# Kernel tuning notes

Hardware: AMD Instinct MI355X
Metric: run time of the kernel (lower is better)

Reference implementation:

```python
import jax, jax.numpy as jnp
import numpy as np
from jax import lax

T, B, NIN, H, NOUT = 256, 64, 256, 2048, 256
DT, TAU, SIGMA = 20.0, 100.0, 0.05
DECAY = DT / TAU                      # alpha in the leaky-Euler update
NOISE_SCALE = SIGMA * float(np.sqrt(2.0 / DECAY))
MAX_INIT_STEPS = 100
ATOL = 0.1


def setup_inputs() -> dict:
    key = jax.random.key(0)
    k1, k2, k3, k4 = jax.random.split(key, 4)
    x = jax.random.normal(k1, (T, B, NIN), dtype=jnp.float32)
    W_ih = jax.random.normal(k2, (H, NIN), dtype=jnp.float32) / np.sqrt(NIN)
    # w_rec_init='diag': strong diagonal plus small random recurrent weights
    W_hh = 0.5 * jnp.eye(H, dtype=jnp.float32) + 0.1 * jax.random.normal(k3, (H, H), dtype=jnp.float32) / np.sqrt(H)
    b = jnp.zeros((H,), dtype=jnp.float32)
    W_out = jax.random.normal(k4, (NOUT, H), dtype=jnp.float32) / np.sqrt(H)
    return {"x": x, "W_ih": W_ih, "W_hh": W_hh, "b": b, "W_out": W_out}


def reference(x, W_ih, W_hh, b, W_out):
    base = jax.random.key(42)

    def cell(h, x_t, k):
        # leaky RNN step: h' = (1-a)h + a*relu(W_ih x + W_hh h + b + noise)
        pre = x_t @ W_ih.T + h @ W_hh.T + b
        pre = pre + NOISE_SCALE * jax.random.normal(k, pre.shape, dtype=pre.dtype)
        return (1.0 - DECAY) * h + DECAY * jax.nn.relu(pre)

    # ---- init_hidden_: up to 100 probe iterations of 2 steps on x[:2, 0:1] ----
    x_probe = x[:2, :1]                       # [2, 1, NIN], broadcasts vs h [B, H]
    h0_init = jnp.zeros((B, H), dtype=x.dtype)

    def init_body(carry, i):
        h0, stable, done = carry
        k = jax.random.fold_in(base, i)
        ka, kb = jax.random.split(k)
        h1 = cell(h0, x_probe[0], ka)
        h2 = cell(h1, x_probe[1], kb)
        close = jnp.max(jnp.abs(h2 - h0)) <= ATOL
        stable_new = jnp.where(done, stable, jnp.where(close, stable + 1, 0))
        trigger = (~done) & close & (stable_new >= 4)   # return pre-update h0
        done_new = done | trigger
        h0_new = jnp.where(done_new, h0, h2)
        return (h0_new, stable_new, done_new), None

    (h0, _, _), _ = lax.scan(init_body, (h0_init, jnp.int32(0), jnp.bool_(False)),
                             jnp.arange(MAX_INIT_STEPS))

    # ---- main unroll over T steps ----
    ks = jax.random.split(jax.random.fold_in(base, 1_000_000), T)

    def step(h, inp):
        x_t, k = inp
        h_new = cell(h, x_t, k)
        return h_new, h_new

    _, hidden = lax.scan(step, h0, (x, ks))   # [T, B, H]
    output = hidden @ W_out.T                 # [T, B, NOUT]
    return output, hidden
```

## Files before the change

kernel.cpp:

```cpp
#include <hip/hip_runtime.h>

typedef unsigned int u32;
typedef unsigned short u16;
typedef __bf16 bf16x8 __attribute__((ext_vector_type(8)));
typedef u16 us8 __attribute__((ext_vector_type(8)));
typedef u32 u32x4 __attribute__((ext_vector_type(4)));
typedef float f32x4 __attribute__((ext_vector_type(4)));

#define T_N 256
#define B_N 64
#define NIN_N 256
#define H_N 2048
#define NOUT_N 256
#define BH (B_N * H_N)
#define OUT_SZ (T_N * B_N * NOUT_N)

#define LDS_WHH_H 0
#define LDS_WHH_L 65536
#define LDS_RBUF  131072
#define LDS_RED   139264
#define LDS_BYTES 139328

struct U2 { u32 x, y; };

__device__ __forceinline__ u32 rotl32(u32 v, int r) { return (v << r) | (v >> (32 - r)); }

__device__ __forceinline__ U2 tf2x32(U2 k, U2 x) {
  u32 ks0 = k.x, ks1 = k.y, ks2 = k.x ^ k.y ^ 0x1BD11BDAu;
  x.x += ks0; x.y += ks1;
#define TFR(a) x.x += x.y; x.y = rotl32(x.y,(a)); x.y ^= x.x;
  TFR(13) TFR(15) TFR(26) TFR(6)
  x.x += ks1; x.y += ks2 + 1u;
  TFR(17) TFR(29) TFR(16) TFR(24)
  x.x += ks2; x.y += ks0 + 2u;
  TFR(13) TFR(15) TFR(26) TFR(6)
  x.x += ks0; x.y += ks1 + 3u;
  TFR(17) TFR(29) TFR(16) TFR(24)
  x.x += ks1; x.y += ks2 + 4u;
  TFR(13) TFR(15) TFR(26) TFR(6)
  x.x += ks2; x.y += ks0 + 5u;
#undef TFR
  return x;
}

__device__ __forceinline__ float jax_normal(u32 bits) {
  float f = __uint_as_float((bits >> 9) | 0x3f800000u) - 1.0f;
  const float lo = -0.99999994f;
  float u = fmaf(f, 2.0f, lo);
  u = fmaxf(u, lo);
  float w = -log1pf(-u * u);
  float p;
  if (w < 5.0f) {
    w = w - 2.5f;
    p =            2.81022636e-08f;
    p = fmaf(p, w, 3.43273939e-07f);
    p = fmaf(p, w, -3.5233877e-06f);
    p = fmaf(p, w, -4.39150654e-06f);
    p = fmaf(p, w, 0.00021858087f);
    p = fmaf(p, w, -0.00125372503f);
    p = fmaf(p, w, -0.00417768164f);
    p = fmaf(p, w, 0.246640727f);
    p = fmaf(p, w, 1.50140941f);
  } else {
    w = sqrtf(w) - 3.0f;
    p =            -0.000200214257f;
    p = fmaf(p, w, 0.000100950558f);
    p = fmaf(p, w, 0.00134934322f);
    p = fmaf(p, w, -0.00367342844f);
    p = fmaf(p, w, 0.00573950773f);
    p = fmaf(p, w, -0.0076224613f);
    p = fmaf(p, w, 0.00943887047f);
    p = fmaf(p, w, 1.00167406f);
    p = fmaf(p, w, 2.83297682f);
  }
  return 1.41421354f * (p * u);
}

__device__ __forceinline__ u16 f2bf(float f) {
  u32 x = __float_as_uint(f);
  u32 r = (x + 0x7FFFu + ((x >> 16) & 1u)) >> 16;
  return (u16)r;
}
__device__ __forceinline__ float bf2f(u16 b) { return __uint_as_float(((u32)b) << 16); }

__device__ __forceinline__ bf16x8 ld8(const u16* p) {
  us8 v = *reinterpret_cast<const us8*>(p);
  return __builtin_bit_cast(bf16x8, v);
}
__device__ __forceinline__ f32x4 mfma16(bf16x8 a, bf16x8 b, f32x4 c) {
  return __builtin_amdgcn_mfma_f32_16x16x32_bf16(a, b, c, 0, 0, 0);
}

__device__ __forceinline__ void st_agent_u16(u16* p, u16 v) {
  __hip_atomic_store(p, v, __ATOMIC_RELAXED, __HIP_MEMORY_SCOPE_AGENT);
}
__device__ __forceinline__ void st_agent_u32(u32* p, u32 v, int order) {
  if (order) __hip_atomic_store(p, v, __ATOMIC_RELEASE, __HIP_MEMORY_SCOPE_AGENT);
  else       __hip_atomic_store(p, v, __ATOMIC_RELAXED, __HIP_MEMORY_SCOPE_AGENT);
}
__device__ __forceinline__ u32 ld_agent_u32(const u32* p) {
  return __hip_atomic_load(p, __ATOMIC_RELAXED, __HIP_MEMORY_SCOPE_AGENT);
}

#define GLD16(AP, V) \
  asm volatile( \
    "global_load_dwordx4 %0, %16, off offset:-4096 sc0 sc1\n\t" \
    "global_load_dwordx4 %1, %16, off sc0 sc1\n\t" \
    "global_load_dwordx4 %2, %17, off offset:-4096 sc0 sc1\n\t" \
    "global_load_dwordx4 %3, %17, off sc0 sc1\n\t" \
    "global_load_dwordx4 %4, %18, off offset:-4096 sc0 sc1\n\t" \
    "global_load_dwordx4 %5, %18, off sc0 sc1\n\t" \
    "global_load_dwordx4 %6, %19, off offset:-4096 sc0 sc1\n\t" \
    "global_load_dwordx4 %7, %19, off sc0 sc1\n\t" \
    "global_load_dwordx4 %8, %20, off offset:-4096 sc0 sc1\n\t" \
    "global_load_dwordx4 %9, %20, off sc0 sc1\n\t" \
    "global_load_dwordx4 %10, %21, off offset:-4096 sc0 sc1\n\t" \
    "global_load_dwordx4 %11, %21, off sc0 sc1\n\t" \
    "global_load_dwordx4 %12, %22, off offset:-4096 sc0 sc1\n\t" \
    "global_load_dwordx4 %13, %22, off sc0 sc1\n\t" \
    "global_load_dwordx4 %14, %23, off offset:-4096 sc0 sc1\n\t" \
    "global_load_dwordx4 %15, %23, off sc0 sc1\n\t" \
    "s_waitcnt vmcnt(0)" \
    : "=&v"(V##0), "=&v"(V##1), "=&v"(V##2), "=&v"(V##3), \
      "=&v"(V##4), "=&v"(V##5), "=&v"(V##6), "=&v"(V##7), \
      "=&v"(V##8), "=&v"(V##9), "=&v"(V##10), "=&v"(V##11), \
      "=&v"(V##12), "=&v"(V##13), "=&v"(V##14), "=&v"(V##15) \
    : "v"(AP + 2048), "v"(AP + 3 * 2048), "v"(AP + 5 * 2048), "v"(AP + 7 * 2048), \
      "v"(AP + 9 * 2048), "v"(AP + 11 * 2048), "v"(AP + 13 * 2048), "v"(AP + 15 * 2048) \
    : "memory")

__global__ void __launch_bounds__(256) pack_b_kernel(const float* __restrict__ W,
    u16* __restrict__ hi, u16* __restrict__ lo, int K, int Cshift) {
  int tid = blockIdx.x * 256 + threadIdx.x;
  int lane = tid & 63;
  size_t tile = tid >> 6;
  int C = 1 << Cshift;
  int jt = (int)(tile >> Cshift), c = (int)(tile & (C - 1));
  int row = jt * 16 + (lane & 15);
  int k0 = c * 32 + (lane >> 4) * 8;
  const float* src = W + (size_t)row * K + k0;
  us8 vh, vl;
#pragma unroll
  for (int j = 0; j < 8; ++j) {
    float w = src[j];
    u16 hb = f2bf(w);
    vh[j] = hb;
    vl[j] = f2bf(w - bf2f(hb));
  }
  *reinterpret_cast<us8*>(hi + tile * 512 + lane * 8) = vh;
  *reinterpret_cast<us8*>(lo + tile * 512 + lane * 8) = vl;
}

__global__ void __launch_bounds__(256) pack_x_kernel(const float* __restrict__ x,
    u16* __restrict__ hi, u16* __restrict__ lo) {
  int tid = blockIdx.x * 256 + threadIdx.x;
  int t = tid >> 11;
  int r = tid & 2047;
  int lane = r & 63, piece = r >> 6;
  int c = piece >> 2, g = piece & 3;
  int row = g * 16 + (lane & 15);
  int k0 = c * 32 + (lane >> 4) * 8;
  const float* src = x + (size_t)t * (B_N * NIN_N) + (size_t)row * NIN_N + k0;
  us8 vh, vl;
#pragma unroll
  for (int j = 0; j < 8; ++j) {
    float w = src[j];
    u16 hb = f2bf(w);
    vh[j] = hb;
    vl[j] = f2bf(w - bf2f(hb));
  }
  size_t off = (size_t)t * 16384 + (size_t)piece * 512 + lane * 8;
  *reinterpret_cast<us8*>(hi + off) = vh;
  *reinterpret_cast<us8*>(lo + off) = vl;
}

__global__ void __launch_bounds__(256) probe_proj(const float* __restrict__ x,
    const float* __restrict__ Wih, const float* __restrict__ bias, float* __restrict__ xpj) {
  int g = blockIdx.x * 256 + threadIdx.x;
  int p = g >> 11, col = g & 2047;
  const float* xr = x + (size_t)p * (B_N * NIN_N);
  const float* wr = Wih + (size_t)col * NIN_N;
  float s = 0.f;
#pragma unroll 4
  for (int k = 0; k < NIN_N; ++k) s = fmaf(xr[k], wr[k], s);
  xpj[p * H_N + col] = s + bias[col];
}

__global__ void __launch_bounds__(256) xproj_gemm(const u16* __restrict__ xp_hi,
    const u16* __restrict__ xp_lo, const u16* __restrict__ wih_hi,
    const u16* __restrict__ wih_lo, const float* __restrict__ bias,
    float* __restrict__ xout) {
  int lane = threadIdx.x & 63, wvq = threadIdx.x >> 6;
  int t = blockIdx.x >> 7, jt16 = blockIdx.x & 127;
  const u16* ah = xp_hi + (size_t)t * 16384 + wvq * 512 + lane * 8;
  const u16* al = xp_lo + (size_t)t * 16384 + wvq * 512 + lane * 8;
  const u16* bh = wih_hi + (size_t)jt16 * 4096 + lane * 8;
  const u16* bl = wih_lo + (size_t)jt16 * 4096 + lane * 8;
  f32x4 z = {0.f, 0.f, 0.f, 0.f};
  f32x4 a0 = z, a1 = z, a2 = z;
#pragma unroll
  for (int c = 0; c < 8; ++c) {
    bf16x8 xh = ld8(ah + c * 2048), xl = ld8(al + c * 2048);
    bf16x8 wh = ld8(bh + c * 512),  wl = ld8(bl + c * 512);
    a0 = mfma16(xh, wh, a0);
    a1 = mfma16(xh, wl, a1);
    a2 = mfma16(xl, wh, a2);
  }
  f32x4 acc = (a0 + a1) + a2;
  int col = jt16 * 16 + (lane & 15);
  int q = lane >> 4;
  float bc = bias[col];
#pragma unroll
  for (int r = 0; r < 4; ++r) {
    int row = wvq * 16 + q * 4 + r;
    xout[(size_t)t * BH + (size_t)row * H_N + col] = acc[r] + bc;
  }
}

__global__ void setup_keys(U2* ka, U2* kb, U2* ks) {
  int i = threadIdx.x;
  U2 base{0u, 42u};
  if (i < 104) {
    U2 ki = tf2x32(base, U2{0u, (u32)i});
    ka[i] = tf2x32(ki, U2{0u, 0u});
    kb[i] = tf2x32(ki, U2{0u, 1u});
  }
  U2 km = tf2x32(base, U2{0u, 1000000u});
  ks[i] = tf2x32(km, U2{0u, (u32)i});
}

__global__ void __launch_bounds__(256) zero_bufs(u32* hx0w, u32* hx0lw, u32* bar) {
  int g = blockIdx.x * 256 + threadIdx.x;
  if (g < BH / 2) { hx0w[g] = 0u; hx0lw[g] = 0u; }
  if (g < 1024) bar[g] = 0u;
}

struct RnnParams {
  const u16 *whh_hi, *whh_lo;
  const float* xpj;
  float* hidden;
  u16 *hx0, *hx1, *hx2, *hxA, *hxB;
  u16 *hx0l, *hx1l, *hx2l;
  const U2 *ka, *kb, *ks;
  u32 *slots, *mslot;
};

__global__ void __launch_bounds__(512) rnn_persistent(RnnParams P) {
  extern __shared__ char smem[];
  u16* lwhh_h = (u16*)(smem + LDS_WHH_H);
  u16* lwhh_l = (u16*)(smem + LDS_WHH_L);
  f32x4* rbuf = (f32x4*)(smem + LDS_RBUF);
  float* red  = (float*)(smem + LDS_RED);

  const int lane = threadIdx.x & 63;
  const int wv = threadIdx.x >> 6;
  const int rg = wv >> 2;
  const int kh = wv & 3;
  const int blk = blockIdx.x;
  const int jt16 = blk & 127;
  const int rh = blk >> 7;
  const int bqg = rh * 2 + rg;
  const int q = lane >> 4;
  const int row = bqg * 16 + q * 4 + kh;
  const int col = jt16 * 16 + (lane & 15);
  const u32 idx = (u32)row * H_N + (u32)col;
  const u32 xoff = ((u32)((col >> 5) * 4 + (row >> 4)) * 64
                    + (u32)(((col >> 3) & 3) * 16 + (row & 15))) * 8 + (u32)(col & 7);

  {
    const us8* sh = (const us8*)(P.whh_hi + (size_t)jt16 * 32768);
    const us8* sl = (const us8*)(P.whh_lo + (size_t)jt16 * 32768);
    us8* dh = (us8*)lwhh_h;
    us8* dl = (us8*)lwhh_l;
#pragma unroll 2
    for (int i = threadIdx.x; i < 4096; i += 512) { dh[i] = sh[i]; dl[i] = sl[i]; }
    __syncthreads();
  }
  const u16* bhp = lwhh_h + kh * 8192 + lane * 8;
  const u16* blp = lwhh_l + kh * 8192 + lane * 8;

  u32 ebar = 0;
  auto bar_cell = [&](bool agg) {
    ++ebar;
    asm volatile("s_waitcnt vmcnt(0)" ::: "memory");
    __syncthreads();
    if (wv == 0) {
      if (lane == 0) {
        if (agg) {
          float m = red[0];
#pragma unroll
          for (int w2 = 1; w2 < 8; ++w2) m = fmaxf(m, red[w2]);
          st_agent_u32(P.mslot + blk, __float_as_uint(m), 0);
        }
        st_agent_u32(P.slots + blk, ebar, 1);
      }
      for (;;) {
        u32 a = ld_agent_u32(P.slots + lane * 4 + 0);
        u32 b = ld_agent_u32(P.slots + lane * 4 + 1);
        u32 c = ld_agent_u32(P.slots + lane * 4 + 2);
        u32 d = ld_agent_u32(P.slots + lane * 4 + 3);
        u32 mn = a < b ? a : b;
        u32 mn2 = c < d ? c : d;
        mn = mn < mn2 ? mn : mn2;
        if (__all(mn >= ebar)) break;
        __builtin_amdgcn_s_sleep(1);
      }
      u32 payload = 0u;
      if (agg) {
        float m = fmaxf(fmaxf(__uint_as_float(ld_agent_u32(P.mslot + lane * 4 + 0)),
                              __uint_as_float(ld_agent_u32(P.mslot + lane * 4 + 1))),
                        fmaxf(__uint_as_float(ld_agent_u32(P.mslot + lane * 4 + 2)),
                              __uint_as_float(ld_agent_u32(P.mslot + lane * 4 + 3))));
#pragma unroll
        for (int o = 32; o >= 1; o >>= 1) m = fmaxf(m, __shfl_down(m, o));
        payload = (m <= 0.1f) ? 1u : 0u;
      }
      if (lane == 0) ((u32*)red)[8] = payload;
    }
    __syncthreads();
  };

  auto reduce_av = [&](f32x4 acc) -> float {
    rbuf[wv * 64 + lane] = acc;
    __syncthreads();
    const float* rb = (const float*)(rbuf + rg * 256);
    return rb[lane * 4 + kh] + rb[256 + lane * 4 + kh]
         + rb[512 + lane * 4 + kh] + rb[768 + lane * 4 + kh];
  };

  auto gemm_hi = [&](const u16* hx_in) -> float {
    const u16* ap = hx_in + bqg * 512 + kh * 32768 + lane * 8;
    u32x4 A0, A1, A2, A3, A4, A5, A6, A7, A8, A9, A10, A11, A12, A13, A14, A15;
    GLD16(ap, A);
    f32x4 z = {0.f, 0.f, 0.f, 0.f};
    f32x4 a0 = z, a1 = z, a2 = z, a3 = z;
#define HSTEP(c, AV) { bf16x8 bh_ = ld8(bhp + (c) * 512); bf16x8 bl_ = ld8(blp + (c) * 512); \
    bf16x8 ah_ = __builtin_bit_cast(bf16x8, AV); \
    if ((c) & 1) { a2 = mfma16(ah_, bh_, a2); a3 = mfma16(ah_, bl_, a3); } \
    else { a0 = mfma16(ah_, bh_, a0); a1 = mfma16(ah_, bl_, a1); } }
    HSTEP(0, A0)  HSTEP(1, A1)  HSTEP(2, A2)  HSTEP(3, A3)
    HSTEP(4, A4)  HSTEP(5, A5)  HSTEP(6, A6)  HSTEP(7, A7)
    HSTEP(8, A8)  HSTEP(9, A9)  HSTEP(10, A10) HSTEP(11, A11)
    HSTEP(12, A12) HSTEP(13, A13) HSTEP(14, A14) HSTEP(15, A15)
#undef HSTEP
    return reduce_av((a0 + a1) + (a2 + a3));
  };

  auto gemm_hilo = [&](const u16* hx_in, const u16* hx_lo) -> float {
    const u16* aph = hx_in + bqg * 512 + kh * 32768 + lane * 8;
    const u16* apl = hx_lo + bqg * 512 + kh * 32768 + lane * 8;
    f32x4 z = {0.f, 0.f, 0.f, 0.f};
    f32x4 a0 = z, a1 = z, a2 = z, a3 = z, a4 = z, a5 = z;
    {
      u32x4 H0, H1, H2, H3, H4, H5, H6, H7, H8, H9, H10, H11, H12, H13, H14, H15;
      GLD16(aph, H);
#define ISTEP(c, AV) { bf16x8 bh_ = ld8(bhp + (c) * 512); bf16x8 bl_ = ld8(blp + (c) * 512); \
      bf16x8 ah_ = __builtin_bit_cast(bf16x8, AV); \
      if ((c) & 1) { a3 = mfma16(ah_, bh_, a3); a4 = mfma16(ah_, bl_, a4); } \
      else { a0 = mfma16(ah_, bh_, a0); a1 = mfma16(ah_, bl_, a1); } }
      ISTEP(0, H0)  ISTEP(1, H1)  ISTEP(2, H2)  ISTEP(3, H3)
      ISTEP(4, H4)  ISTEP(5, H5)  ISTEP(6, H6)  ISTEP(7, H7)
      ISTEP(8, H8)  ISTEP(9, H9)  ISTEP(10, H10) ISTEP(11, H11)
      ISTEP(12, H12) ISTEP(13, H13) ISTEP(14, H14) ISTEP(15, H15)
#undef ISTEP
    }
    {
      u32x4 L0, L1, L2, L3, L4, L5, L6, L7, L8, L9, L10, L11, L12, L13, L14, L15;
      GLD16(apl, L);
#define LSTEP(c, AV) { bf16x8 bh_ = ld8(bhp + (c) * 512); \
      bf16x8 al_ = __builtin_bit_cast(bf16x8, AV); \
      if ((c) & 1) { a5 = mfma16(al_, bh_, a5); } \
      else { a2 = mfma16(al_, bh_, a2); } }
      LSTEP(0, L0)  LSTEP(1, L1)  LSTEP(2, L2)  LSTEP(3, L3)
      LSTEP(4, L4)  LSTEP(5, L5)  LSTEP(6, L6)  LSTEP(7, L7)
      LSTEP(8, L8)  LSTEP(9, L9)  LSTEP(10, L10) LSTEP(11, L11)
      LSTEP(12, L12) LSTEP(13, L13) LSTEP(14, L14) LSTEP(15, L15)
#undef LSTEP
    }
    return reduce_av(((a0 + a1) + (a2 + a3)) + (a4 + a5));
  };

  auto make_noise = [&](U2 key) -> float {
    U2 o = tf2x32(key, U2{0u, idx});
    return jax_normal(o.x ^ o.y);
  };

  const float NS = 0.15811388300841897f;
  const float xv0 = P.xpj[col];
  const float xv1 = P.xpj[H_N + col];

  u16* hxs[3]  = {P.hx0, P.hx1, P.hx2};
  u16* hxls[3] = {P.hx0l, P.hx1l, P.hx2l};
  int i0 = 0, i1 = 1, i2 = 2;
  float hp0 = 0.f;
  int stable = 0;
  float nzA = make_noise(P.ka[0]);
  float nzB = 0.f;

#pragma unroll 1
  for (int it = 0; it < 100; ++it) {
    float av = gemm_hilo(hxs[i0], hxls[i0]);
    float pre = av + xv0 + NS * nzA;
    float hp1 = 0.8f * hp0 + 0.2f * fmaxf(pre, 0.f);
    { u16 hb = f2bf(hp1);
      st_agent_u16(hxs[i1] + xoff, hb);
      st_agent_u16(hxls[i1] + xoff, f2bf(hp1 - bf2f(hb))); }
    nzB = make_noise(P.kb[it]);
    bar_cell(false);

    av = gemm_hilo(hxs[i1], hxls[i1]);
    pre = av + xv1 + NS * nzB;
    float hp2 = 0.8f * hp1 + 0.2f * fmaxf(pre, 0.f);
    { u16 hb = f2bf(hp2);
      st_agent_u16(hxs[i2] + xoff, hb);
      st_agent_u16(hxls[i2] + xoff, f2bf(hp2 - bf2f(hb))); }
    float lmax = fabsf(hp2 - hp0);
#pragma unroll
    for (int off = 32; off >= 1; off >>= 1)
      lmax = fmaxf(lmax, __shfl_down(lmax, off));
    if (lane == 0) red[wv] = lmax;
    nzA = make_noise(P.ka[it + 1]);
    bar_cell(true);

    bool close = (((u32*)red)[8] & 1u) != 0u;
    if (close) {
      if (++stable >= 4) break;
    } else stable = 0;
    int tmp = i0; i0 = i2; i2 = tmp;
    hp0 = hp2;
  }

  float nzS = make_noise(P.ks[0]);
  float xv = P.hidden[idx];
  float hp = hp0;
#pragma unroll 1
  for (int t = 0; t < T_N; ++t) {
    const u16* hin = (t == 0) ? hxs[i0] : (((t - 1) & 1) ? P.hxB : P.hxA);
    float av = gemm_hi(hin);
    float pre = av + xv + NS * nzS;
    float hn = 0.8f * hp + 0.2f * fmaxf(pre, 0.f);
    hp = hn;
    P.hidden[(size_t)t * BH + idx] = hn;
    st_agent_u16(((t & 1) ? P.hxB : P.hxA) + xoff, f2bf(hn));
    if (t != T_N - 1) {
      xv = P.hidden[(size_t)(t + 1) * BH + idx];
      nzS = make_noise(P.ks[t + 1]);
      bar_cell(false);
    }
  }
}

__global__ void __launch_bounds__(256) out_gemm(const float* __restrict__ hidden,
    const u16* __restrict__ wo_hi, const u16* __restrict__ wo_lo, float* __restrict__ out) {
  int lane = threadIdx.x & 63, wv = threadIdx.x >> 6;
  int mb = blockIdx.x * 64 + wv * 16;
  int arow = mb + (lane & 15);
  int q = lane >> 4;
  f32x4 acc[16];
#pragma unroll
  for (int n = 0; n < 16; ++n) acc[n] = {0.f, 0.f, 0.f, 0.f};
  const float* ap = hidden + (size_t)arow * H_N + q * 8;
#pragma unroll 2
  for (int c = 0; c < 64; ++c) {
    const float4* a4 = reinterpret_cast<const float4*>(ap + c * 32);
    float4 f0 = a4[0], f1 = a4[1];
    us8 av;
    av[0] = f2bf(f0.x); av[1] = f2bf(f0.y); av[2] = f2bf(f0.z); av[3] = f2bf(f0.w);
    av[4] = f2bf(f1.x); av[5] = f2bf(f1.y); av[6] = f2bf(f1.z); av[7] = f2bf(f1.w);
    bf16x8 a = __builtin_bit_cast(bf16x8, av);
#pragma unroll
    for (int n = 0; n < 16; ++n) {
      bf16x8 bh = ld8(wo_hi + ((size_t)(n * 64 + c) * 64 + lane) * 8);
      bf16x8 bl = ld8(wo_lo + ((size_t)(n * 64 + c) * 64 + lane) * 8);
      acc[n] = mfma16(a, bh, acc[n]);
      acc[n] = mfma16(a, bl, acc[n]);
    }
  }
#pragma unroll
  for (int n = 0; n < 16; ++n)
#pragma unroll
    for (int r = 0; r < 4; ++r)
      out[(size_t)(mb + q * 4 + r) * NOUT_N + n * 16 + (lane & 15)] = acc[n][r];
}

extern "C" void kernel_launch(void* const* d_in, const int* in_sizes, int n_in,
                              void* d_out, int out_size, void* d_ws, size_t ws_size,
                              hipStream_t stream) {
  const float* x = (const float*)d_in[0];
  const float* W_ih = (const float*)d_in[1];
  const float* W_hh = (const float*)d_in[2];
  const float* bias = (const float*)d_in[3];
  const float* W_out = (const float*)d_in[4];
  float* out = (float*)d_out;

  char* ws = (char*)d_ws;
  size_t off = 0;
  auto alloc = [&](size_t bytes) -> void* {
    void* p = ws + off;
    off += (bytes + 255) & ~(size_t)255;
    return p;
  };
  u16* whh_hi = (u16*)alloc(8388608);
  u16* whh_lo = (u16*)alloc(8388608);
  u16* wih_hi = (u16*)alloc(1048576);
  u16* wih_lo = (u16*)alloc(1048576);
  u16* wout_hi = (u16*)alloc(1048576);
  u16* wout_lo = (u16*)alloc(1048576);
  u16* xp_hi = (u16*)alloc(8388608);
  u16* xp_lo = (u16*)alloc(8388608);
  float* xpj = (float*)alloc(16384);
  u16* hx0 = (u16*)alloc(262144);
  u16* hx1 = (u16*)alloc(262144);
  u16* hx2 = (u16*)alloc(262144);
  u16* hxA = (u16*)alloc(262144);
  u16* hxB = (u16*)alloc(262144);
  u16* hx0l = (u16*)alloc(262144);
  u16* hx1l = (u16*)alloc(262144);
  u16* hx2l = (u16*)alloc(262144);
  U2* ka = (U2*)alloc(832);
  U2* kb = (U2*)alloc(832);
  U2* ks = (U2*)alloc(2048);
  u32* bar = (u32*)alloc(4096);

  float* hidden = out + OUT_SZ;

  hipLaunchKernelGGL(pack_b_kernel, dim3(2048), dim3(256), 0, stream, W_hh, whh_hi, whh_lo, 2048, 6);
  hipLaunchKernelGGL(pack_b_kernel, dim3(256), dim3(256), 0, stream, W_ih, wih_hi, wih_lo, 256, 3);
  hipLaunchKernelGGL(pack_b_kernel, dim3(256), dim3(256), 0, stream, W_out, wout_hi, wout_lo, 2048, 6);
  hipLaunchKernelGGL(pack_x_kernel, dim3(2048), dim3(256), 0, stream, x, xp_hi, xp_lo);
  hipLaunchKernelGGL(probe_proj, dim3(16), dim3(256), 0, stream, x, W_ih, bias, xpj);
  hipLaunchKernelGGL(setup_keys, dim3(1), dim3(256), 0, stream, ka, kb, ks);
  hipLaunchKernelGGL(zero_bufs, dim3(256), dim3(256), 0, stream, (u32*)hx0, (u32*)hx0l, bar);
  hipLaunchKernelGGL(xproj_gemm, dim3(32768), dim3(256), 0, stream, xp_hi, xp_lo, wih_hi, wih_lo, bias, hidden);

  RnnParams P;
  P.whh_hi = whh_hi; P.whh_lo = whh_lo;
  P.xpj = xpj;
  P.hidden = hidden;
  P.hx0 = hx0; P.hx1 = hx1; P.hx2 = hx2; P.hxA = hxA; P.hxB = hxB;
  P.hx0l = hx0l; P.hx1l = hx1l; P.hx2l = hx2l;
  P.ka = ka; P.kb = kb; P.ks = ks;
  P.slots = bar; P.mslot = bar + 256;

  static bool attr_set = false;
  if (!attr_set) {
    hipFuncSetAttribute((const void*)rnn_persistent,
                        hipFuncAttributeMaxDynamicSharedMemorySize, LDS_BYTES);
    attr_set = true;
  }

  void* kargs[] = {(void*)&P};
  hipLaunchCooperativeKernel((const void*)rnn_persistent, dim3(256), dim3(512), kargs, LDS_BYTES, stream);

  hipLaunchKernelGGL(out_gemm, dim3(256), dim3(256), 0, stream, hidden, wout_hi, wout_lo, out);
}
```

Before: 5.200 ms.

## Keep W_hh slices in registers, narrow barrier to half-grid, defer hidden stores

The recurrent weight tile moves from LDS into per-thread registers (32 bf16x8 vectors), which removes the LDS staging buffers and the per-step LDS reads of B. The main-loop barrier now waits only on the 128 blocks of the same row half (rh) using vector acquire loads, instead of on all 256 blocks. The hidden-state store and next-step xproj load are moved after the barrier so they overlap the wait. This adds register pressure (launch_bounds 512,2) and depends on the row-half dependency being correct.

```diff
diff --git a/kernel.cpp b/kernel.cpp
--- a/kernel.cpp
+++ b/kernel.cpp
@@ -4,6 +4,7 @@
 typedef unsigned short u16;
 typedef __bf16 bf16x8 __attribute__((ext_vector_type(8)));
 typedef u16 us8 __attribute__((ext_vector_type(8)));
+typedef u32 u32x2 __attribute__((ext_vector_type(2)));
 typedef u32 u32x4 __attribute__((ext_vector_type(4)));
 typedef float f32x4 __attribute__((ext_vector_type(4)));
 
@@ -14,12 +15,6 @@
 #define NOUT_N 256
 #define BH (B_N * H_N)
 #define OUT_SZ (T_N * B_N * NOUT_N)
-
-#define LDS_WHH_H 0
-#define LDS_WHH_L 65536
-#define LDS_RBUF  131072
-#define LDS_RED   139264
-#define LDS_BYTES 139328
 
 struct U2 { u32 x, y; };
 
@@ -245,12 +240,9 @@
   u32 *slots, *mslot;
 };
 
-__global__ void __launch_bounds__(512) rnn_persistent(RnnParams P) {
-  extern __shared__ char smem[];
-  u16* lwhh_h = (u16*)(smem + LDS_WHH_H);
-  u16* lwhh_l = (u16*)(smem + LDS_WHH_L);
-  f32x4* rbuf = (f32x4*)(smem + LDS_RBUF);
-  float* red  = (float*)(smem + LDS_RED);
+__global__ void __launch_bounds__(512, 2) rnn_persistent(RnnParams P) {
+  __shared__ f32x4 rbuf[512];
+  __shared__ float red[16];
 
   const int lane = threadIdx.x & 63;
   const int wv = threadIdx.x >> 6;
@@ -267,17 +259,16 @@
   const u32 xoff = ((u32)((col >> 5) * 4 + (row >> 4)) * 64
                     + (u32)(((col >> 3) & 3) * 16 + (row & 15))) * 8 + (u32)(col & 7);
 
+  bf16x8 Bh[16], Bl[16];
   {
-    const us8* sh = (const us8*)(P.whh_hi + (size_t)jt16 * 32768);
-    const us8* sl = (const us8*)(P.whh_lo + (size_t)jt16 * 32768);
-    us8* dh = (us8*)lwhh_h;
-    us8* dl = (us8*)lwhh_l;
-#pragma unroll 2
-    for (int i = threadIdx.x; i < 4096; i += 512) { dh[i] = sh[i]; dl[i] = sl[i]; }
-    __syncthreads();
-  }
-  const u16* bhp = lwhh_h + kh * 8192 + lane * 8;
-  const u16* blp = lwhh_l + kh * 8192 + lane * 8;
+    const u16* gbh = P.whh_hi + (size_t)jt16 * 32768 + kh * 8192 + lane * 8;
+    const u16* gbl = P.whh_lo + (size_t)jt16 * 32768 + kh * 8192 + lane * 8;
+#pragma unroll
+    for (int c = 0; c < 16; ++c) {
+      Bh[c] = ld8(gbh + c * 512);
+      Bl[c] = ld8(gbl + c * 512);
+    }
+  }
 
   u32 ebar = 0;
   auto bar_cell = [&](bool agg) {
@@ -294,28 +285,36 @@
         }
         st_agent_u32(P.slots + blk, ebar, 1);
       }
-      for (;;) {
-        u32 a = ld_agent_u32(P.slots + lane * 4 + 0);
-        u32 b = ld_agent_u32(P.slots + lane * 4 + 1);
-        u32 c = ld_agent_u32(P.slots + lane * 4 + 2);
-        u32 d = ld_agent_u32(P.slots + lane * 4 + 3);
-        u32 mn = a < b ? a : b;
-        u32 mn2 = c < d ? c : d;
-        mn = mn < mn2 ? mn : mn2;
-        if (__all(mn >= ebar)) break;
-        __builtin_amdgcn_s_sleep(1);
-      }
-      u32 payload = 0u;
       if (agg) {
+        const u32* ps = P.slots + lane * 4;
+        for (;;) {
+          u32x4 pr;
+          asm volatile("global_load_dwordx4 %0, %1, off sc0 sc1\n\ts_waitcnt vmcnt(0)"
+                       : "=&v"(pr) : "v"(ps) : "memory");
+          u32 mn = pr.x < pr.y ? pr.x : pr.y;
+          u32 mn2 = pr.z < pr.w ? pr.z : pr.w;
+          mn = mn < mn2 ? mn : mn2;
+          if (__all(mn >= ebar)) break;
+          __builtin_amdgcn_s_sleep(1);
+        }
         float m = fmaxf(fmaxf(__uint_as_float(ld_agent_u32(P.mslot + lane * 4 + 0)),
                               __uint_as_float(ld_agent_u32(P.mslot + lane * 4 + 1))),
                         fmaxf(__uint_as_float(ld_agent_u32(P.mslot + lane * 4 + 2)),
                               __uint_as_float(ld_agent_u32(P.mslot + lane * 4 + 3))));
 #pragma unroll
         for (int o = 32; o >= 1; o >>= 1) m = fmaxf(m, __shfl_down(m, o));
-        payload = (m <= 0.1f) ? 1u : 0u;
+        if (lane == 0) ((u32*)red)[8] = (m <= 0.1f) ? 1u : 0u;
+      } else {
+        const u32* ps = P.slots + rh * 128 + lane * 2;
+        for (;;) {
+          u32x2 pr;
+          asm volatile("global_load_dwordx2 %0, %1, off sc0 sc1\n\ts_waitcnt vmcnt(0)"
+                       : "=&v"(pr) : "v"(ps) : "memory");
+          u32 mn = pr.x < pr.y ? pr.x : pr.y;
+          if (__all(mn >= ebar)) break;
+          __builtin_amdgcn_s_sleep(1);
+        }
       }
-      if (lane == 0) ((u32*)red)[8] = payload;
     }
     __syncthreads();
   };
@@ -334,10 +333,9 @@
     GLD16(ap, A);
     f32x4 z = {0.f, 0.f, 0.f, 0.f};
     f32x4 a0 = z, a1 = z, a2 = z, a3 = z;
-#define HSTEP(c, AV) { bf16x8 bh_ = ld8(bhp + (c) * 512); bf16x8 bl_ = ld8(blp + (c) * 512); \
-    bf16x8 ah_ = __builtin_bit_cast(bf16x8, AV); \
-    if ((c) & 1) { a2 = mfma16(ah_, bh_, a2); a3 = mfma16(ah_, bl_, a3); } \
-    else { a0 = mfma16(ah_, bh_, a0); a1 = mfma16(ah_, bl_, a1); } }
+#define HSTEP(c, AV) { bf16x8 ah_ = __builtin_bit_cast(bf16x8, AV); \
+    if ((c) & 1) { a2 = mfma16(ah_, Bh[c], a2); a3 = mfma16(ah_, Bl[c], a3); } \
+    else { a0 = mfma16(ah_, Bh[c], a0); a1 = mfma16(ah_, Bl[c], a1); } }
     HSTEP(0, A0)  HSTEP(1, A1)  HSTEP(2, A2)  HSTEP(3, A3)
     HSTEP(4, A4)  HSTEP(5, A5)  HSTEP(6, A6)  HSTEP(7, A7)
     HSTEP(8, A8)  HSTEP(9, A9)  HSTEP(10, A10) HSTEP(11, A11)
@@ -354,10 +352,9 @@
     {
       u32x4 H0, H1, H2, H3, H4, H5, H6, H7, H8, H9, H10, H11, H12, H13, H14, H15;
       GLD16(aph, H);
-#define ISTEP(c, AV) { bf16x8 bh_ = ld8(bhp + (c) * 512); bf16x8 bl_ = ld8(blp + (c) * 512); \
-      bf16x8 ah_ = __builtin_bit_cast(bf16x8, AV); \
-      if ((c) & 1) { a3 = mfma16(ah_, bh_, a3); a4 = mfma16(ah_, bl_, a4); } \
-      else { a0 = mfma16(ah_, bh_, a0); a1 = mfma16(ah_, bl_, a1); } }
+#define ISTEP(c, AV) { bf16x8 ah_ = __builtin_bit_cast(bf16x8, AV); \
+      if ((c) & 1) { a3 = mfma16(ah_, Bh[c], a3); a4 = mfma16(ah_, Bl[c], a4); } \
+      else { a0 = mfma16(ah_, Bh[c], a0); a1 = mfma16(ah_, Bl[c], a1); } }
       ISTEP(0, H0)  ISTEP(1, H1)  ISTEP(2, H2)  ISTEP(3, H3)
       ISTEP(4, H4)  ISTEP(5, H5)  ISTEP(6, H6)  ISTEP(7, H7)
       ISTEP(8, H8)  ISTEP(9, H9)  ISTEP(10, H10) ISTEP(11, H11)
@@ -367,10 +364,9 @@
     {
       u32x4 L0, L1, L2, L3, L4, L5, L6, L7, L8, L9, L10, L11, L12, L13, L14, L15;
       GLD16(apl, L);
-#define LSTEP(c, AV) { bf16x8 bh_ = ld8(bhp + (c) * 512); \
-      bf16x8 al_ = __builtin_bit_cast(bf16x8, AV); \
-      if ((c) & 1) { a5 = mfma16(al_, bh_, a5); } \
-      else { a2 = mfma16(al_, bh_, a2); } }
+#define LSTEP(c, AV) { bf16x8 al_ = __builtin_bit_cast(bf16x8, AV); \
+      if ((c) & 1) { a5 = mfma16(al_, Bh[c], a5); } \
+      else { a2 = mfma16(al_, Bh[c], a2); } }
       LSTEP(0, L0)  LSTEP(1, L1)  LSTEP(2, L2)  LSTEP(3, L3)
       LSTEP(4, L4)  LSTEP(5, L5)  LSTEP(6, L6)  LSTEP(7, L7)
       LSTEP(8, L8)  LSTEP(9, L9)  LSTEP(10, L10) LSTEP(11, L11)
@@ -440,12 +436,14 @@
     float pre = av + xv + NS * nzS;
     float hn = 0.8f * hp + 0.2f * fmaxf(pre, 0.f);
     hp = hn;
-    P.hidden[(size_t)t * BH + idx] = hn;
     st_agent_u16(((t & 1) ? P.hxB : P.hxA) + xoff, f2bf(hn));
     if (t != T_N - 1) {
-      xv = P.hidden[(size_t)(t + 1) * BH + idx];
       nzS = make_noise(P.ks[t + 1]);
       bar_cell(false);
+      P.hidden[(size_t)t * BH + idx] = hn;
+      xv = P.hidden[(size_t)(t + 1) * BH + idx];
+    } else {
+      P.hidden[(size_t)t * BH + idx] = hn;
     }
   }
 }
@@ -542,15 +540,8 @@
   P.ka = ka; P.kb = kb; P.ks = ks;
   P.slots = bar; P.mslot = bar + 256;
 
-  static bool attr_set = false;
-  if (!attr_set) {
-    hipFuncSetAttribute((const void*)rnn_persistent,
-                        hipFuncAttributeMaxDynamicSharedMemorySize, LDS_BYTES);
-    attr_set = true;
-  }
-
   void* kargs[] = {(void*)&P};
-  hipLaunchCooperativeKernel((const void*)rnn_persistent, dim3(256), dim3(512), kargs, LDS_BYTES, stream);
+  hipLaunchCooperativeKernel((const void*)rnn_persistent, dim3(256), dim3(512), kargs, 0, stream);
 
   hipLaunchKernelGGL(out_gemm, dim3(256), dim3(256), 0, stream, hidden, wout_hi, wout_lo, out);
 }
```

Measured after the change: 5.388 ms. 1.04x slower.

## Replace global barriers with per-dependency flag polling and triple-buffered hidden state

Applied to the files above, without the earlier changes.

Swaps the full grid barrier between recurrent steps for point-to-point readiness flags. Each wave polls only the 32 blocks whose hidden-state slice it reads, and the scan rotates over three buffers so writers cannot overwrite data still being read. The reduction barrier stays only where the convergence max is needed, and barrier slot polling now uses a single vectorised load. This is meant to cut barrier latency and let blocks run ahead of one another, at the cost of subtler memory-ordering correctness.

```diff
diff --git a/kernel.cpp b/kernel.cpp
--- a/kernel.cpp
+++ b/kernel.cpp
@@ -239,10 +239,12 @@
   const u16 *whh_hi, *whh_lo;
   const float* xpj;
   float* hidden;
-  u16 *hx0, *hx1, *hx2, *hxA, *hxB;
+  u16 *hx0, *hx1, *hx2;
   u16 *hx0l, *hx1l, *hx2l;
+  u16 *hxS0, *hxS1, *hxS2;
   const U2 *ka, *kb, *ks;
   u32 *slots, *mslot;
+  u32 *initflag, *scanflag;
 };
 
 __global__ void __launch_bounds__(512) rnn_persistent(RnnParams P) {
@@ -279,43 +281,57 @@
   const u16* bhp = lwhh_h + kh * 8192 + lane * 8;
   const u16* blp = lwhh_l + kh * 8192 + lane * 8;
 
+  const u32* fl_init = P.initflag + rh * 128 + kh * 32;
+  const u32* fl_scan = P.scanflag + rh * 128 + kh * 32;
+
+  auto poll32 = [&](const u32* fl, u32 need) {
+    const u32* p = fl + (lane & 31);
+    for (;;) {
+      u32 v;
+      asm volatile("global_load_dword %0, %1, off sc0 sc1\n\ts_waitcnt vmcnt(0)"
+                   : "=v"(v) : "v"(p) : "memory");
+      if (__all(v >= need)) break;
+      __builtin_amdgcn_s_sleep(1);
+    }
+  };
+
+  auto publish = [&](u32* flagarr, u32 val) {
+    asm volatile("s_waitcnt vmcnt(0)" ::: "memory");
+    __syncthreads();
+    if (threadIdx.x == 0) st_agent_u32(flagarr + blk, val, 1);
+  };
+
   u32 ebar = 0;
-  auto bar_cell = [&](bool agg) {
+  auto bar_agg = [&]() {
     ++ebar;
     asm volatile("s_waitcnt vmcnt(0)" ::: "memory");
     __syncthreads();
     if (wv == 0) {
       if (lane == 0) {
-        if (agg) {
-          float m = red[0];
-#pragma unroll
-          for (int w2 = 1; w2 < 8; ++w2) m = fmaxf(m, red[w2]);
-          st_agent_u32(P.mslot + blk, __float_as_uint(m), 0);
-        }
+        float m = red[0];
+#pragma unroll
+        for (int w2 = 1; w2 < 8; ++w2) m = fmaxf(m, red[w2]);
+        st_agent_u32(P.mslot + blk, __float_as_uint(m), 0);
         st_agent_u32(P.slots + blk, ebar, 1);
       }
+      const u32* ps = P.slots + lane * 4;
       for (;;) {
-        u32 a = ld_agent_u32(P.slots + lane * 4 + 0);
-        u32 b = ld_agent_u32(P.slots + lane * 4 + 1);
-        u32 c = ld_agent_u32(P.slots + lane * 4 + 2);
-        u32 d = ld_agent_u32(P.slots + lane * 4 + 3);
-        u32 mn = a < b ? a : b;
-        u32 mn2 = c < d ? c : d;
+        u32x4 pr;
+        asm volatile("global_load_dwordx4 %0, %1, off sc0 sc1\n\ts_waitcnt vmcnt(0)"
+                     : "=&v"(pr) : "v"(ps) : "memory");
+        u32 mn = pr.x < pr.y ? pr.x : pr.y;
+        u32 mn2 = pr.z < pr.w ? pr.z : pr.w;
         mn = mn < mn2 ? mn : mn2;
         if (__all(mn >= ebar)) break;
         __builtin_amdgcn_s_sleep(1);
       }
-      u32 payload = 0u;
-      if (agg) {
-        float m = fmaxf(fmaxf(__uint_as_float(ld_agent_u32(P.mslot + lane * 4 + 0)),
-                              __uint_as_float(ld_agent_u32(P.mslot + lane * 4 + 1))),
-                        fmaxf(__uint_as_float(ld_agent_u32(P.mslot + lane * 4 + 2)),
-                              __uint_as_float(ld_agent_u32(P.mslot + lane * 4 + 3))));
-#pragma unroll
-        for (int o = 32; o >= 1; o >>= 1) m = fmaxf(m, __shfl_down(m, o));
-        payload = (m <= 0.1f) ? 1u : 0u;
-      }
-      if (lane == 0) ((u32*)red)[8] = payload;
+      float m = fmaxf(fmaxf(__uint_as_float(ld_agent_u32(P.mslot + lane * 4 + 0)),
+                            __uint_as_float(ld_agent_u32(P.mslot + lane * 4 + 1))),
+                      fmaxf(__uint_as_float(ld_agent_u32(P.mslot + lane * 4 + 2)),
+                            __uint_as_float(ld_agent_u32(P.mslot + lane * 4 + 3))));
+#pragma unroll
+      for (int o = 32; o >= 1; o >>= 1) m = fmaxf(m, __shfl_down(m, o));
+      if (lane == 0) ((u32*)red)[8] = (m <= 0.1f) ? 1u : 0u;
     }
     __syncthreads();
   };
@@ -405,8 +421,9 @@
     { u16 hb = f2bf(hp1);
       st_agent_u16(hxs[i1] + xoff, hb);
       st_agent_u16(hxls[i1] + xoff, f2bf(hp1 - bf2f(hb))); }
+    publish(P.initflag, (u32)(it + 1));
     nzB = make_noise(P.kb[it]);
-    bar_cell(false);
+    poll32(fl_init, (u32)(it + 1));
 
     av = gemm_hilo(hxs[i1], hxls[i1]);
     pre = av + xv1 + NS * nzB;
@@ -420,7 +437,7 @@
       lmax = fmaxf(lmax, __shfl_down(lmax, off));
     if (lane == 0) red[wv] = lmax;
     nzA = make_noise(P.ka[it + 1]);
-    bar_cell(true);
+    bar_agg();
 
     bool close = (((u32*)red)[8] & 1u) != 0u;
     if (close) {
@@ -430,22 +447,25 @@
     hp0 = hp2;
   }
 
+  u16* bufs[3] = {P.hxS0, P.hxS1, P.hxS2};
+  st_agent_u16(bufs[0] + xoff, f2bf(hp0));
+  publish(P.scanflag, 1u);
   float nzS = make_noise(P.ks[0]);
   float xv = P.hidden[idx];
   float hp = hp0;
 #pragma unroll 1
   for (int t = 0; t < T_N; ++t) {
-    const u16* hin = (t == 0) ? hxs[i0] : (((t - 1) & 1) ? P.hxB : P.hxA);
-    float av = gemm_hi(hin);
+    poll32(fl_scan, (u32)(t + 1));
+    float av = gemm_hi(bufs[t % 3]);
     float pre = av + xv + NS * nzS;
     float hn = 0.8f * hp + 0.2f * fmaxf(pre, 0.f);
     hp = hn;
     P.hidden[(size_t)t * BH + idx] = hn;
-    st_agent_u16(((t & 1) ? P.hxB : P.hxA) + xoff, f2bf(hn));
     if (t != T_N - 1) {
+      st_agent_u16(bufs[(t + 1) % 3] + xoff, f2bf(hn));
+      publish(P.scanflag, (u32)(t + 2));
+      nzS = make_noise(P.ks[t + 1]);
       xv = P.hidden[(size_t)(t + 1) * BH + idx];
-      nzS = make_noise(P.ks[t + 1]);
-      bar_cell(false);
     }
   }
 }
@@ -512,11 +532,12 @@
   u16* hx0 = (u16*)alloc(262144);
   u16* hx1 = (u16*)alloc(262144);
   u16* hx2 = (u16*)alloc(262144);
-  u16* hxA = (u16*)alloc(262144);
-  u16* hxB = (u16*)alloc(262144);
   u16* hx0l = (u16*)alloc(262144);
   u16* hx1l = (u16*)alloc(262144);
   u16* hx2l = (u16*)alloc(262144);
+  u16* hxS0 = (u16*)alloc(262144);
+  u16* hxS1 = (u16*)alloc(262144);
+  u16* hxS2 = (u16*)alloc(262144);
   U2* ka = (U2*)alloc(832);
   U2* kb = (U2*)alloc(832);
   U2* ks = (U2*)alloc(2048);
@@ -537,10 +558,12 @@
   P.whh_hi = whh_hi; P.whh_lo = whh_lo;
   P.xpj = xpj;
   P.hidden = hidden;
-  P.hx0 = hx0; P.hx1 = hx1; P.hx2 = hx2; P.hxA = hxA; P.hxB = hxB;
+  P.hx0 = hx0; P.hx1 = hx1; P.hx2 = hx2;
   P.hx0l = hx0l; P.hx1l = hx1l; P.hx2l = hx2l;
+  P.hxS0 = hxS0; P.hxS1 = hxS1; P.hxS2 = hxS2;
   P.ka = ka; P.kb = kb; P.ks = ks;
   P.slots = bar; P.mslot = bar + 256;
+  P.initflag = bar + 512; P.scanflag = bar + 768;
 
   static bool attr_set = false;
   if (!attr_set) {
```

Result: faster. 4.955 ms (-4.7%).
